# Kernel tuning notes

Measured on AMD Instinct MI355X. Metric: run time of the kernel, lower is better.

## Reference

```python
import jax, jax.numpy as jnp
import numpy as np

N = 100000   # nodes (single ntype)
R = 3        # relations
E = 500000   # edges per relation
H = 4        # attention heads
F = 64       # out_feat per head
IN = 256     # in_feat
NEG_SLOPE = 0.2  # DGL GATConv default


def setup_inputs() -> dict:
    key = jax.random.key(0)
    ks = jax.random.split(key, 7)
    x = jax.random.normal(ks[0], (N, IN), jnp.float32)
    src = jax.random.randint(ks[1], (R, E), 0, N, dtype=jnp.int32)
    dst = jax.random.randint(ks[2], (R, E), 0, N, dtype=jnp.int32)
    W = jax.random.normal(ks[3], (R, IN, H * F), jnp.float32) / np.sqrt(IN).astype(np.float32)
    attn_l = jax.random.normal(ks[4], (R, H, F), jnp.float32) * 0.1
    attn_r = jax.random.normal(ks[5], (R, H, F), jnp.float32) * 0.1
    bias = jnp.zeros((R, H * F), jnp.float32)
    return {"x": x, "W": W, "attn_l": attn_l, "attn_r": attn_r, "bias": bias,
            "src": src, "dst": dst}


def _gat_relation(x, W_r, al_r, ar_r, b_r, src_r, dst_r):
    # projection: [N, H, F]
    z = (x @ W_r).reshape(N, H, F)
    # per-node attention logits: [N, H]
    el = jnp.sum(z * al_r, axis=-1)
    er = jnp.sum(z * ar_r, axis=-1)
    # edge scores: [E, H]
    e = jax.nn.leaky_relu(el[src_r] + er[dst_r], negative_slope=NEG_SLOPE)
    # segment softmax over incoming edges of each dst node
    m = jax.ops.segment_max(e, dst_r, num_segments=N)      # [N, H]
    ee = jnp.exp(e - m[dst_r])                              # [E, H]
    den = jax.ops.segment_sum(ee, dst_r, num_segments=N)   # [N, H]
    alpha = ee / den[dst_r]                                 # [E, H]
    # weighted scatter-aggregate: [N, H, F]
    rst = jax.ops.segment_sum(z[src_r] * alpha[:, :, None], dst_r, num_segments=N)
    return rst + b_r.reshape(1, H, F)


def reference(x, W, attn_l, attn_r, bias, src, dst):
    # HeteroGraphConv aggregates relations targeting the same ntype with 'sum'
    out = jnp.zeros((N, H, F), x.dtype)
    for r in range(R):
        out = out + _gat_relation(x, W[r], attn_l[r], attn_r[r], bias[r], src[r], dst[r])
    # RelGATConvLayer._apply: activation(h.view(-1, out_feat*num_heads)); dropout=0
    return jax.nn.elu(out.reshape(N, H * F))
```

## Files before the change

kernel.cpp:

```cpp
#include <hip/hip_runtime.h>
#include <hip/hip_bf16.h>


#define RN 100000
#define RE 500000
#define RH 4
#define RIN 256
#define RR 3
#define RHF 256
#define NE3 (RR * RE)
#define N3  (RR * RN)

typedef __attribute__((ext_vector_type(8))) short short8;
typedef __attribute__((ext_vector_type(4))) float f32x4;

static __device__ __forceinline__ float b2f(unsigned short u) {
  return __uint_as_float(((unsigned int)u) << 16);
}
static __device__ __forceinline__ unsigned short f2b(float f) {
  unsigned int u = __float_as_uint(f);
  u += 0x7FFF + ((u >> 16) & 1);
  return (unsigned short)(u >> 16);
}

__global__ __launch_bounds__(256) void rgat_convx(
    const float* __restrict__ x, unsigned short* __restrict__ xb) {
  const size_t i = ((size_t)blockIdx.x * 256 + threadIdx.x) * 4;
  if (i >= (size_t)RN * RIN) return;
  const float4 v = *(const float4*)(x + i);
  ushort4 o;
  o.x = f2b(v.x); o.y = f2b(v.y); o.z = f2b(v.z); o.w = f2b(v.w);
  *(ushort4*)(xb + i) = o;
}

__global__ __launch_bounds__(256) void rgat_convw(
    const float* __restrict__ W, unsigned short* __restrict__ wbt) {
  const int o = blockIdx.x * 256 + threadIdx.x;
  if (o >= RR * RIN * RHF) return;
  const int r = o / (RIN * RHF);
  const int rem = o - r * (RIN * RHF);
  const int n = rem >> 8;
  const int k = rem & 255;
  wbt[o] = f2b(W[r * (RIN * RHF) + k * RHF + n]);
}

__global__ __launch_bounds__(256) void rgat_gemm_bf16(
    const unsigned short* __restrict__ xb, const unsigned short* __restrict__ wbt,
    unsigned short* __restrict__ zb, const float* __restrict__ al,
    const float* __restrict__ ar, float* __restrict__ el,
    float* __restrict__ er) {
  __shared__ unsigned short As[128 * 32];
  __shared__ unsigned short Bs[128 * 32];
  const int tid = threadIdx.x;
  const int lane = tid & 63, wid = tid >> 6;
  const int wr = wid >> 1, wc = wid & 1;
  const int m0 = blockIdx.x * 128;
  const int n0 = blockIdx.y * 128;
  const int r  = blockIdx.z;

  f32x4 acc[4][4] = {};
  const unsigned short* Bbase = wbt + (size_t)r * (RIN * RHF);

  for (int k0 = 0; k0 < RIN; k0 += 32) {
#pragma unroll
    for (int i = 0; i < 2; ++i) {
      const int c = wid * 128 + i * 64 + lane;
      const int row = c >> 2, c4 = c & 3;
      const unsigned short* ga = xb + (size_t)(m0 + row) * RIN + k0 + c4 * 8;
      __builtin_amdgcn_global_load_lds(
          (const __attribute__((address_space(1))) void*)ga,
          (__attribute__((address_space(3))) void*)(As + (wid * 128 + i * 64) * 8),
          16, 0, 0);
      const unsigned short* gb = Bbase + (size_t)(n0 + row) * RIN + k0 + c4 * 8;
      __builtin_amdgcn_global_load_lds(
          (const __attribute__((address_space(1))) void*)gb,
          (__attribute__((address_space(3))) void*)(Bs + (wid * 128 + i * 64) * 8),
          16, 0, 0);
    }
    asm volatile("s_waitcnt vmcnt(0)" ::: "memory");
    __syncthreads();

    short8 af[4], bfr[4];
#pragma unroll
    for (int mi = 0; mi < 4; ++mi)
      af[mi] = *(const short8*)(As + ((wr * 64 + mi * 16 + (lane & 15)) * 32 + (lane >> 4) * 8));
#pragma unroll
    for (int ni = 0; ni < 4; ++ni)
      bfr[ni] = *(const short8*)(Bs + ((wc * 64 + ni * 16 + (lane & 15)) * 32 + (lane >> 4) * 8));
#pragma unroll
    for (int mi = 0; mi < 4; ++mi)
#pragma unroll
      for (int ni = 0; ni < 4; ++ni)
        acc[mi][ni] = __builtin_amdgcn_mfma_f32_16x16x32_bf16(af[mi], bfr[ni], acc[mi][ni], 0, 0, 0);
    __syncthreads();
  }

  const int head = blockIdx.y * 2 + wc;
  float alv[4], arv[4];
#pragma unroll
  for (int ni = 0; ni < 4; ++ni) {
    alv[ni] = al[r * RHF + head * 64 + ni * 16 + (lane & 15)];
    arv[ni] = ar[r * RHF + head * 64 + ni * 16 + (lane & 15)];
  }

  const int mbase = m0 + wr * 64;
#pragma unroll
  for (int mi = 0; mi < 4; ++mi) {
#pragma unroll
    for (int q = 0; q < 4; ++q) {
      const int m = mbase + mi * 16 + (lane >> 4) * 4 + q;
      float pl = 0.f, pr = 0.f;
#pragma unroll
      for (int ni = 0; ni < 4; ++ni) {
        pl += acc[mi][ni][q] * alv[ni];
        pr += acc[mi][ni][q] * arv[ni];
      }
#pragma unroll
      for (int off = 1; off < 16; off <<= 1) {
        pl += __shfl_xor(pl, off);
        pr += __shfl_xor(pr, off);
      }
      if (m < RN) {
        if ((lane & 15) == 0) {
          el[(size_t)(r * (size_t)RN + m) * RH + head] = pl;
          er[(size_t)(r * (size_t)RN + m) * RH + head] = pr;
        }
        unsigned short* zrow = zb + (size_t)r * ((size_t)RN * RHF) + (size_t)m * RHF
                               + n0 + wc * 64 + (lane & 15);
#pragma unroll
        for (int ni = 0; ni < 4; ++ni) zrow[ni * 16] = f2b(acc[mi][ni][q]);
      }
    }
  }
}

__global__ __launch_bounds__(256) void rgat_hist(
    const int* __restrict__ dst, int* __restrict__ deg2) {
  const int i = blockIdx.x * 256 + threadIdx.x;
  if (i >= NE3) return;
  const int r = i / RE;
  atomicAdd(&deg2[dst[i] * RR + r], 1);
}

__global__ __launch_bounds__(256) void rgat_scan1(
    const int* __restrict__ deg, int* __restrict__ offs, int* __restrict__ bsum) {
  __shared__ int sh[256];
  const int tid = threadIdx.x;
  const int base = blockIdx.x * 1024 + tid * 4;
  int v[4]; int s = 0;
#pragma unroll
  for (int j = 0; j < 4; ++j) {
    v[j] = (base + j < N3) ? deg[base + j] : 0;
    s += v[j];
  }
  sh[tid] = s;
  __syncthreads();
  for (int off = 1; off < 256; off <<= 1) {
    int t = (tid >= off) ? sh[tid - off] : 0;
    __syncthreads();
    sh[tid] += t;
    __syncthreads();
  }
  int run = sh[tid] - s;
  if (tid == 255) bsum[blockIdx.x] = sh[255];
#pragma unroll
  for (int j = 0; j < 4; ++j) {
    if (base + j < N3) offs[base + j] = run;
    run += v[j];
  }
}

__global__ __launch_bounds__(512) void rgat_scan2(int* __restrict__ bsum, int nb) {
  __shared__ int sh[512];
  const int tid = threadIdx.x;
  const int v = (tid < nb) ? bsum[tid] : 0;
  sh[tid] = v;
  __syncthreads();
  for (int off = 1; off < 512; off <<= 1) {
    int t = (tid >= off) ? sh[tid - off] : 0;
    __syncthreads();
    sh[tid] += t;
    __syncthreads();
  }
  if (tid < nb) bsum[tid] = sh[tid] - v;
}

__global__ __launch_bounds__(256) void rgat_scan3(
    int* __restrict__ offs, const int* __restrict__ bsum) {
  const int base = blockIdx.x * 1024 + threadIdx.x * 4;
  const int b = bsum[blockIdx.x];
#pragma unroll
  for (int j = 0; j < 4; ++j)
    if (base + j < N3) offs[base + j] += b;
}

__global__ __launch_bounds__(256) void rgat_scatter(
    const int* __restrict__ src, const int* __restrict__ dst,
    const float* __restrict__ el, const float* __restrict__ er,
    int* __restrict__ offs2, int* __restrict__ czoff,
    float4* __restrict__ cee) {
  const int i = blockIdx.x * 256 + threadIdx.x;
  if (i >= NE3) return;
  const int r = i / RE;
  const int s = src[i];
  const int d = dst[i];
  const int pos = atomicAdd(&offs2[d * RR + r], 1);
  const float4 elv = *(const float4*)(el + (size_t)(r * (size_t)RN + s) * RH);
  const float4 erv = *(const float4*)(er + (size_t)(r * (size_t)RN + d) * RH);
  float e0 = elv.x + erv.x, e1 = elv.y + erv.y, e2 = elv.z + erv.z, e3 = elv.w + erv.w;
  e0 = e0 > 0.f ? e0 : 0.2f * e0;
  e1 = e1 > 0.f ? e1 : 0.2f * e1;
  e2 = e2 > 0.f ? e2 : 0.2f * e2;
  e3 = e3 > 0.f ? e3 : 0.2f * e3;
  czoff[pos] = r * RN + s;
  cee[pos] = make_float4(__expf(e0), __expf(e1), __expf(e2), __expf(e3));
}

__global__ __launch_bounds__(256) void rgat_norm(
    float4* __restrict__ cee, const int* __restrict__ deg2,
    const int* __restrict__ offs2) {
  const int key = blockIdx.x * 256 + threadIdx.x;
  if (key >= N3) return;
  const int d = deg2[key];
  const int end = offs2[key];
  float s0 = 0.f, s1 = 0.f, s2 = 0.f, s3 = 0.f;
  for (int p = end - d; p < end; ++p) {
    const float4 v = cee[p];
    s0 += v.x; s1 += v.y; s2 += v.z; s3 += v.w;
  }
  const float i0 = s0 > 0.f ? 1.f / s0 : 0.f;
  const float i1 = s1 > 0.f ? 1.f / s1 : 0.f;
  const float i2 = s2 > 0.f ? 1.f / s2 : 0.f;
  const float i3 = s3 > 0.f ? 1.f / s3 : 0.f;
  for (int p = end - d; p < end; ++p) {
    float4 v = cee[p];
    v.x *= i0; v.y *= i1; v.z *= i2; v.w *= i3;
    cee[p] = v;
  }
}

__global__ __launch_bounds__(256) void rgat_aggregate(
    const unsigned short* __restrict__ zb, const int* __restrict__ czoff,
    const float* __restrict__ alpha, const int* __restrict__ deg2,
    const int* __restrict__ offs2, const float* __restrict__ bias,
    float* __restrict__ out) {
  __shared__ float shn[4][RHF];
  const int n = blockIdx.x;
  const int tid = threadIdx.x;
  const int wid = tid >> 6, lane = tid & 63;
  const int hw = lane >> 5;
  const int sub = lane & 31;
  const int hwid = wid * 2 + hw;
  const int h = sub >> 3;
  const int c = sub * 8;

  const int k0 = n * RR;
  const int start = offs2[k0] - deg2[k0];
  const int dm = offs2[k0 + 2] - start;

  float acc[8] = {};
  const unsigned short* zB = zb + c;

  for (int base = 0; base < dm; base += 16) {
    int ss[2]; float aa[2];
#pragma unroll
    for (int j = 0; j < 2; ++j) {
      const int t = base + j * 8 + hwid;
      const int tc = t < dm ? t : dm - 1;
      const int p = start + tc;
      ss[j] = czoff[p];
      const float af = alpha[p * 4 + h];
      aa[j] = t < dm ? af : 0.f;
    }
    short8 zv[2];
#pragma unroll
    for (int j = 0; j < 2; ++j)
      zv[j] = *(const short8*)(zB + (size_t)ss[j] * RHF);
#pragma unroll
    for (int j = 0; j < 2; ++j) {
      const float a = aa[j];
#pragma unroll
      for (int k = 0; k < 8; ++k)
        acc[k] += a * b2f((unsigned short)zv[j][k]);
    }
  }

#pragma unroll
  for (int k = 0; k < 8; ++k) acc[k] += __shfl_xor(acc[k], 32);

  if (lane < 32) {
    *(float4*)&shn[wid][c]     = make_float4(acc[0], acc[1], acc[2], acc[3]);
    *(float4*)&shn[wid][c + 4] = make_float4(acc[4], acc[5], acc[6], acc[7]);
  }
  __syncthreads();

  const int col = tid;
  float v = shn[0][col] + shn[1][col] + shn[2][col] + shn[3][col]
          + bias[col] + bias[RHF + col] + bias[2 * RHF + col];
  v = v > 0.f ? v : (__expf(v) - 1.f);
  out[(size_t)n * RHF + col] = v;
}

extern "C" void kernel_launch(void* const* d_in, const int* in_sizes, int n_in,
                              void* d_out, int out_size, void* d_ws, size_t ws_size,
                              hipStream_t stream) {
  const float* x    = (const float*)d_in[0];
  const float* W    = (const float*)d_in[1];
  const float* al   = (const float*)d_in[2];
  const float* ar   = (const float*)d_in[3];
  const float* bias = (const float*)d_in[4];
  const int*   src  = (const int*)d_in[5];
  const int*   dst  = (const int*)d_in[6];
  float* out = (float*)d_out;

  char* p = (char*)d_ws;
  unsigned short* xb  = (unsigned short*)p; p += (size_t)RN * RIN * 2;
  unsigned short* wbt = (unsigned short*)p; p += (size_t)RR * RIN * RHF * 2;
  unsigned short* zb  = (unsigned short*)p; p += (size_t)RR * RN * RHF * 2;
  float* el    = (float*)p;  p += (size_t)RR * RN * RH * 4;
  float* er    = (float*)p;  p += (size_t)RR * RN * RH * 4;
  int* deg2    = (int*)p;    p += (size_t)N3 * 4;
  int* offs2   = (int*)p;    p += (size_t)N3 * 4;
  int* czoff   = (int*)p;    p += (size_t)NE3 * 4;
  float4* cee  = (float4*)p; p += (size_t)NE3 * 16;
  int* bsum    = (int*)p;    p += 2048;

  const int NB1 = (N3 + 1023) / 1024;

  hipMemsetAsync(deg2, 0, (size_t)N3 * 4, stream);

  rgat_convx<<<(RN * RIN / 4 + 255) / 256, 256, 0, stream>>>(x, xb);
  rgat_convw<<<(RR * RIN * RHF + 255) / 256, 256, 0, stream>>>(W, wbt);

  rgat_hist<<<(NE3 + 255) / 256, 256, 0, stream>>>(dst, deg2);
  rgat_scan1<<<NB1, 256, 0, stream>>>(deg2, offs2, bsum);
  rgat_scan2<<<1, 512, 0, stream>>>(bsum, NB1);
  rgat_scan3<<<NB1, 256, 0, stream>>>(offs2, bsum);

  rgat_gemm_bf16<<<dim3((RN + 127) / 128, RHF / 128, RR), 256, 0, stream>>>(
      xb, wbt, zb, al, ar, el, er);

  rgat_scatter<<<(NE3 + 255) / 256, 256, 0, stream>>>(src, dst, el, er, offs2,
                                                      czoff, cee);

  rgat_norm<<<(N3 + 255) / 256, 256, 0, stream>>>(cee, deg2, offs2);

  rgat_aggregate<<<RN, 256, 0, stream>>>(zb, czoff, (const float*)cee, deg2,
                                         offs2, bias, out);
}
```

Before: 619.2 us.

## Store attention logits and edge weights in fp16 and transpose GEMM output tiles

The GEMM swaps operand roles so each lane holds four consecutive output features. That allows packed bf16 conversion and 8-byte vector stores of z, and el/er reductions that need fewer shuffles. The el/er logits and the per-edge exp/alpha buffer are stored as fp16 instead of fp32, halving their memory traffic in the scatter, norm and aggregate kernels. This costs precision in the unnormalised exp values, which can overflow or lose accuracy for large logits.

```diff
diff --git a/kernel.cpp b/kernel.cpp
--- a/kernel.cpp
+++ b/kernel.cpp
@@ -21,6 +21,17 @@
   unsigned int u = __float_as_uint(f);
   u += 0x7FFF + ((u >> 16) & 1);
   return (unsigned short)(u >> 16);
+}
+static __device__ __forceinline__ float h2f(unsigned short u) {
+  return (float)__builtin_bit_cast(_Float16, u);
+}
+static __device__ __forceinline__ unsigned short f2h(float f) {
+  return __builtin_bit_cast(unsigned short, (_Float16)f);
+}
+static __device__ __forceinline__ unsigned int cvt_pk_bf16(float lo, float hi) {
+  unsigned int r;
+  asm("v_cvt_pk_bf16_f32 %0, %1, %2" : "=v"(r) : "v"(lo), "v"(hi));
+  return r;
 }
 
 __global__ __launch_bounds__(256) void rgat_convx(
@@ -47,8 +58,8 @@
 __global__ __launch_bounds__(256) void rgat_gemm_bf16(
     const unsigned short* __restrict__ xb, const unsigned short* __restrict__ wbt,
     unsigned short* __restrict__ zb, const float* __restrict__ al,
-    const float* __restrict__ ar, float* __restrict__ el,
-    float* __restrict__ er) {
+    const float* __restrict__ ar, unsigned short* __restrict__ elh,
+    unsigned short* __restrict__ erh) {
   __shared__ unsigned short As[128 * 32];
   __shared__ unsigned short Bs[128 * 32];
   const int tid = threadIdx.x;
@@ -80,56 +91,54 @@
     asm volatile("s_waitcnt vmcnt(0)" ::: "memory");
     __syncthreads();
 
-    short8 af[4], bfr[4];
-#pragma unroll
-    for (int mi = 0; mi < 4; ++mi)
-      af[mi] = *(const short8*)(As + ((wr * 64 + mi * 16 + (lane & 15)) * 32 + (lane >> 4) * 8));
-#pragma unroll
-    for (int ni = 0; ni < 4; ++ni)
-      bfr[ni] = *(const short8*)(Bs + ((wc * 64 + ni * 16 + (lane & 15)) * 32 + (lane >> 4) * 8));
-#pragma unroll
-    for (int mi = 0; mi < 4; ++mi)
-#pragma unroll
-      for (int ni = 0; ni < 4; ++ni)
-        acc[mi][ni] = __builtin_amdgcn_mfma_f32_16x16x32_bf16(af[mi], bfr[ni], acc[mi][ni], 0, 0, 0);
-    __syncthreads();
-  }
-
-  const int head = blockIdx.y * 2 + wc;
-  float alv[4], arv[4];
-#pragma unroll
-  for (int ni = 0; ni < 4; ++ni) {
-    alv[ni] = al[r * RHF + head * 64 + ni * 16 + (lane & 15)];
-    arv[ni] = ar[r * RHF + head * 64 + ni * 16 + (lane & 15)];
-  }
-
-  const int mbase = m0 + wr * 64;
-#pragma unroll
-  for (int mi = 0; mi < 4; ++mi) {
-#pragma unroll
-    for (int q = 0; q < 4; ++q) {
-      const int m = mbase + mi * 16 + (lane >> 4) * 4 + q;
-      float pl = 0.f, pr = 0.f;
-#pragma unroll
-      for (int ni = 0; ni < 4; ++ni) {
-        pl += acc[mi][ni][q] * alv[ni];
-        pr += acc[mi][ni][q] * arv[ni];
-      }
-#pragma unroll
-      for (int off = 1; off < 16; off <<= 1) {
-        pl += __shfl_xor(pl, off);
-        pr += __shfl_xor(pr, off);
-      }
-      if (m < RN) {
-        if ((lane & 15) == 0) {
-          el[(size_t)(r * (size_t)RN + m) * RH + head] = pl;
-          er[(size_t)(r * (size_t)RN + m) * RH + head] = pr;
-        }
-        unsigned short* zrow = zb + (size_t)r * ((size_t)RN * RHF) + (size_t)m * RHF
-                               + n0 + wc * 64 + (lane & 15);
-#pragma unroll
-        for (int ni = 0; ni < 4; ++ni) zrow[ni * 16] = f2b(acc[mi][ni][q]);
-      }
+    short8 wf[4], xf[4];
+#pragma unroll
+    for (int ci = 0; ci < 4; ++ci)
+      wf[ci] = *(const short8*)(Bs + ((wr * 64 + ci * 16 + (lane & 15)) * 32 + (lane >> 4) * 8));
+#pragma unroll
+    for (int xi = 0; xi < 4; ++xi)
+      xf[xi] = *(const short8*)(As + ((wc * 64 + xi * 16 + (lane & 15)) * 32 + (lane >> 4) * 8));
+#pragma unroll
+    for (int ci = 0; ci < 4; ++ci)
+#pragma unroll
+      for (int xi = 0; xi < 4; ++xi)
+        acc[ci][xi] = __builtin_amdgcn_mfma_f32_16x16x32_bf16(wf[ci], xf[xi], acc[ci][xi], 0, 0, 0);
+    __syncthreads();
+  }
+
+  const int head = blockIdx.y * 2 + wr;
+  const int g4 = (lane >> 4) * 4;
+  float alv[4][4], arv[4][4];
+#pragma unroll
+  for (int ci = 0; ci < 4; ++ci) {
+    const float4 a4 = *(const float4*)(al + r * RHF + head * 64 + ci * 16 + g4);
+    const float4 b4 = *(const float4*)(ar + r * RHF + head * 64 + ci * 16 + g4);
+    alv[ci][0] = a4.x; alv[ci][1] = a4.y; alv[ci][2] = a4.z; alv[ci][3] = a4.w;
+    arv[ci][0] = b4.x; arv[ci][1] = b4.y; arv[ci][2] = b4.z; arv[ci][3] = b4.w;
+  }
+
+#pragma unroll
+  for (int xi = 0; xi < 4; ++xi) {
+    const int node = m0 + wc * 64 + xi * 16 + (lane & 15);
+    unsigned short* zrow = zb + (size_t)r * ((size_t)RN * RHF) + (size_t)node * RHF
+                           + n0 + wr * 64 + g4;
+    float pl = 0.f, pr = 0.f;
+#pragma unroll
+    for (int ci = 0; ci < 4; ++ci) {
+      const f32x4 a = acc[ci][xi];
+      uint2 pk;
+      pk.x = cvt_pk_bf16(a[0], a[1]);
+      pk.y = cvt_pk_bf16(a[2], a[3]);
+      if (node < RN) *(uint2*)(zrow + ci * 16) = pk;
+      pl += a[0] * alv[ci][0] + a[1] * alv[ci][1] + a[2] * alv[ci][2] + a[3] * alv[ci][3];
+      pr += a[0] * arv[ci][0] + a[1] * arv[ci][1] + a[2] * arv[ci][2] + a[3] * arv[ci][3];
+    }
+    pl += __shfl_xor(pl, 16); pl += __shfl_xor(pl, 32);
+    pr += __shfl_xor(pr, 16); pr += __shfl_xor(pr, 32);
+    if (lane < 16 && node < RN) {
+      const size_t key = (size_t)r * RN + node;
+      elh[key * RH + head] = f2h(pl);
+      erh[key * RH + head] = f2h(pr);
     }
   }
 }
@@ -196,28 +205,34 @@
 
 __global__ __launch_bounds__(256) void rgat_scatter(
     const int* __restrict__ src, const int* __restrict__ dst,
-    const float* __restrict__ el, const float* __restrict__ er,
+    const unsigned short* __restrict__ elh, const unsigned short* __restrict__ erh,
     int* __restrict__ offs2, int* __restrict__ czoff,
-    float4* __restrict__ cee) {
+    unsigned short* __restrict__ ceeh) {
   const int i = blockIdx.x * 256 + threadIdx.x;
   if (i >= NE3) return;
   const int r = i / RE;
   const int s = src[i];
   const int d = dst[i];
   const int pos = atomicAdd(&offs2[d * RR + r], 1);
-  const float4 elv = *(const float4*)(el + (size_t)(r * (size_t)RN + s) * RH);
-  const float4 erv = *(const float4*)(er + (size_t)(r * (size_t)RN + d) * RH);
-  float e0 = elv.x + erv.x, e1 = elv.y + erv.y, e2 = elv.z + erv.z, e3 = elv.w + erv.w;
+  const uint2 eu = *(const uint2*)(elh + ((size_t)r * RN + s) * RH);
+  const uint2 ru = *(const uint2*)(erh + ((size_t)r * RN + d) * RH);
+  float e0 = h2f((unsigned short)eu.x) + h2f((unsigned short)ru.x);
+  float e1 = h2f((unsigned short)(eu.x >> 16)) + h2f((unsigned short)(ru.x >> 16));
+  float e2 = h2f((unsigned short)eu.y) + h2f((unsigned short)ru.y);
+  float e3 = h2f((unsigned short)(eu.y >> 16)) + h2f((unsigned short)(ru.y >> 16));
   e0 = e0 > 0.f ? e0 : 0.2f * e0;
   e1 = e1 > 0.f ? e1 : 0.2f * e1;
   e2 = e2 > 0.f ? e2 : 0.2f * e2;
   e3 = e3 > 0.f ? e3 : 0.2f * e3;
   czoff[pos] = r * RN + s;
-  cee[pos] = make_float4(__expf(e0), __expf(e1), __expf(e2), __expf(e3));
+  uint2 o;
+  o.x = (unsigned int)f2h(__expf(e0)) | ((unsigned int)f2h(__expf(e1)) << 16);
+  o.y = (unsigned int)f2h(__expf(e2)) | ((unsigned int)f2h(__expf(e3)) << 16);
+  *(uint2*)(ceeh + (size_t)pos * 4) = o;
 }
 
 __global__ __launch_bounds__(256) void rgat_norm(
-    float4* __restrict__ cee, const int* __restrict__ deg2,
+    unsigned short* __restrict__ ceeh, const int* __restrict__ deg2,
     const int* __restrict__ offs2) {
   const int key = blockIdx.x * 256 + threadIdx.x;
   if (key >= N3) return;
@@ -225,23 +240,31 @@
   const int end = offs2[key];
   float s0 = 0.f, s1 = 0.f, s2 = 0.f, s3 = 0.f;
   for (int p = end - d; p < end; ++p) {
-    const float4 v = cee[p];
-    s0 += v.x; s1 += v.y; s2 += v.z; s3 += v.w;
+    const uint2 v = *(const uint2*)(ceeh + (size_t)p * 4);
+    s0 += h2f((unsigned short)v.x);
+    s1 += h2f((unsigned short)(v.x >> 16));
+    s2 += h2f((unsigned short)v.y);
+    s3 += h2f((unsigned short)(v.y >> 16));
   }
   const float i0 = s0 > 0.f ? 1.f / s0 : 0.f;
   const float i1 = s1 > 0.f ? 1.f / s1 : 0.f;
   const float i2 = s2 > 0.f ? 1.f / s2 : 0.f;
   const float i3 = s3 > 0.f ? 1.f / s3 : 0.f;
   for (int p = end - d; p < end; ++p) {
-    float4 v = cee[p];
-    v.x *= i0; v.y *= i1; v.z *= i2; v.w *= i3;
-    cee[p] = v;
+    uint2 v = *(const uint2*)(ceeh + (size_t)p * 4);
+    const float a0 = h2f((unsigned short)v.x) * i0;
+    const float a1 = h2f((unsigned short)(v.x >> 16)) * i1;
+    const float a2 = h2f((unsigned short)v.y) * i2;
+    const float a3 = h2f((unsigned short)(v.y >> 16)) * i3;
+    v.x = (unsigned int)f2h(a0) | ((unsigned int)f2h(a1) << 16);
+    v.y = (unsigned int)f2h(a2) | ((unsigned int)f2h(a3) << 16);
+    *(uint2*)(ceeh + (size_t)p * 4) = v;
   }
 }
 
 __global__ __launch_bounds__(256) void rgat_aggregate(
     const unsigned short* __restrict__ zb, const int* __restrict__ czoff,
-    const float* __restrict__ alpha, const int* __restrict__ deg2,
+    const unsigned short* __restrict__ ceeh, const int* __restrict__ deg2,
     const int* __restrict__ offs2, const float* __restrict__ bias,
     float* __restrict__ out) {
   __shared__ float shn[4][RHF];
@@ -269,7 +292,7 @@
       const int tc = t < dm ? t : dm - 1;
       const int p = start + tc;
       ss[j] = czoff[p];
-      const float af = alpha[p * 4 + h];
+      const float af = h2f(ceeh[(size_t)p * 4 + h]);
       aa[j] = t < dm ? af : 0.f;
     }
     short8 zv[2];
@@ -314,15 +337,15 @@
   float* out = (float*)d_out;
 
   char* p = (char*)d_ws;
-  unsigned short* xb  = (unsigned short*)p; p += (size_t)RN * RIN * 2;
-  unsigned short* wbt = (unsigned short*)p; p += (size_t)RR * RIN * RHF * 2;
-  unsigned short* zb  = (unsigned short*)p; p += (size_t)RR * RN * RHF * 2;
-  float* el    = (float*)p;  p += (size_t)RR * RN * RH * 4;
-  float* er    = (float*)p;  p += (size_t)RR * RN * RH * 4;
+  unsigned short* xb   = (unsigned short*)p; p += (size_t)RN * RIN * 2;
+  unsigned short* wbt  = (unsigned short*)p; p += (size_t)RR * RIN * RHF * 2;
+  unsigned short* zb   = (unsigned short*)p; p += (size_t)RR * RN * RHF * 2;
+  unsigned short* elh  = (unsigned short*)p; p += (size_t)N3 * RH * 2;
+  unsigned short* erh  = (unsigned short*)p; p += (size_t)N3 * RH * 2;
   int* deg2    = (int*)p;    p += (size_t)N3 * 4;
   int* offs2   = (int*)p;    p += (size_t)N3 * 4;
   int* czoff   = (int*)p;    p += (size_t)NE3 * 4;
-  float4* cee  = (float4*)p; p += (size_t)NE3 * 16;
+  unsigned short* ceeh = (unsigned short*)p; p += (size_t)NE3 * RH * 2;
   int* bsum    = (int*)p;    p += 2048;
 
   const int NB1 = (N3 + 1023) / 1024;
@@ -338,13 +361,12 @@
   rgat_scan3<<<NB1, 256, 0, stream>>>(offs2, bsum);
 
   rgat_gemm_bf16<<<dim3((RN + 127) / 128, RHF / 128, RR), 256, 0, stream>>>(
-      xb, wbt, zb, al, ar, el, er);
-
-  rgat_scatter<<<(NE3 + 255) / 256, 256, 0, stream>>>(src, dst, el, er, offs2,
-                                                      czoff, cee);
-
-  rgat_norm<<<(N3 + 255) / 256, 256, 0, stream>>>(cee, deg2, offs2);
-
-  rgat_aggregate<<<RN, 256, 0, stream>>>(zb, czoff, (const float*)cee, deg2,
-                                         offs2, bias, out);
-}
+      xb, wbt, zb, al, ar, elh, erh);
+
+  rgat_scatter<<<(NE3 + 255) / 256, 256, 0, stream>>>(src, dst, elh, erh, offs2,
+                                                      czoff, ceeh);
+
+  rgat_norm<<<(N3 + 255) / 256, 256, 0, stream>>>(ceeh, deg2, offs2);
+
+  rgat_aggregate<<<RN, 256, 0, stream>>>(zb, czoff, ceeh, deg2, offs2, bias, out);
+}
```

After: 603.5 us. 1.03x faster.
